# Kernel optimization log

Hardware: AMD Instinct MI355X
Metric: run time of the kernel (lower is better)

## Reference

```python
import jax, jax.numpy as jnp
import numpy as np

B, S, T, D, H, DF = 2, 2048, 2048, 1024, 16, 4096
DK = D // H
EPS = 1e-5


def _linear_params(key, d_in, d_out):
    kw, kb = jax.random.split(key)
    s = 1.0 / np.sqrt(d_in)
    W = jax.random.uniform(kw, (d_out, d_in), jnp.float32, -s, s)
    b = jax.random.uniform(kb, (d_out,), jnp.float32, -s, s)
    return W, b


def setup_inputs() -> dict:
    key = jax.random.key(0)
    ks = jax.random.split(key, 16)
    inp = {}
    inp['x'] = jax.random.normal(ks[0], (B, S, D), jnp.float32)
    inp['enc_out'] = jax.random.normal(ks[1], (B, T, D), jnp.float32)
    inp['src_mask'] = jnp.ones((B, 1, 1, T), jnp.int32)
    inp['tgt_mask'] = jnp.tril(jnp.ones((S, S), jnp.int32))[None, None, :, :]
    # self-attn params
    for i, nm in enumerate(['q1', 'k1', 'v1', 'o1']):
        W, b = _linear_params(ks[2 + i], D, D)
        inp['W' + nm], inp['b' + nm] = W, b
    # cross-attn params
    for i, nm in enumerate(['q2', 'k2', 'v2', 'o2']):
        W, b = _linear_params(ks[6 + i], D, D)
        inp['W' + nm], inp['b' + nm] = W, b
    # FFN
    inp['Wf1'], inp['bf1'] = _linear_params(ks[10], D, DF)
    inp['Wf2'], inp['bf2'] = _linear_params(ks[11], DF, D)
    # LayerNorms
    for i in (1, 2, 3):
        inp[f'g{i}'] = jnp.ones((D,), jnp.float32)
        inp[f'be{i}'] = jnp.zeros((D,), jnp.float32)
    return inp


def _lin(x, W, b):
    return x @ W.T + b


def _ln(x, g, b):
    mu = jnp.mean(x, -1, keepdims=True)
    var = jnp.mean(jnp.square(x - mu), -1, keepdims=True)
    return (x - mu) * jax.lax.rsqrt(var + EPS) * g + b


def _mha(q_in, k_in, v_in, Wq, bq, Wk, bk, Wv, bv, Wo, bo, mask):
    Bq = q_in.shape[0]
    q = _lin(q_in, Wq, bq).reshape(Bq, -1, H, DK).transpose(0, 2, 1, 3)
    k = _lin(k_in, Wk, bk).reshape(Bq, -1, H, DK).transpose(0, 2, 1, 3)
    v = _lin(v_in, Wv, bv).reshape(Bq, -1, H, DK).transpose(0, 2, 1, 3)
    scores = jnp.einsum('bhqd,bhkd->bhqk', q, k) / np.sqrt(DK)
    scores = jnp.where(mask == 0, -jnp.inf, scores)
    attn = jax.nn.softmax(scores, axis=-1)
    out = jnp.einsum('bhqk,bhkd->bhqd', attn, v)
    out = out.transpose(0, 2, 1, 3).reshape(Bq, -1, H * DK)
    return _lin(out, Wo, bo)


def reference(x, enc_out, src_mask, tgt_mask,
              Wq1, bq1, Wk1, bk1, Wv1, bv1, Wo1, bo1,
              Wq2, bq2, Wk2, bk2, Wv2, bv2, Wo2, bo2,
              Wf1, bf1, Wf2, bf2,
              g1, be1, g2, be2, g3, be3):
    out = _mha(x, x, x, Wq1, bq1, Wk1, bk1, Wv1, bv1, Wo1, bo1, tgt_mask)
    x = _ln(x + out, g1, be1)
    out = _mha(x, enc_out, enc_out, Wq2, bq2, Wk2, bk2, Wv2, bv2, Wo2, bo2, src_mask)
    x = _ln(x + out, g2, be2)
    ff = _lin(jax.nn.relu(_lin(x, Wf1, bf1)), Wf2, bf2)
    return _ln(x + ff, g3, be3)
```

## Files before the change

### kernel.cpp

```cpp
#include <hip/hip_runtime.h>


typedef __bf16 bf16_t;
typedef bf16_t  bf16x8 __attribute__((ext_vector_type(8)));
typedef float   f32x4  __attribute__((ext_vector_type(4)));
typedef unsigned short ushort_t;
typedef ushort_t u16x8 __attribute__((ext_vector_type(8)));
typedef ushort_t u16x4 __attribute__((ext_vector_type(4)));

__device__ __forceinline__ float b2f(ushort_t u) {
    union { unsigned u; float f; } x; x.u = ((unsigned)u) << 16; return x.f;
}
__device__ __forceinline__ ushort_t f2b(float f) {
    union { float f; unsigned u; } x; x.f = f;
    unsigned r = x.u + 0x7fffu + ((x.u >> 16) & 1u);
    return (ushort_t)(r >> 16);
}
__device__ __forceinline__ unsigned pk2(float lo, float hi) {
    union { float f; unsigned u; } a, b; a.f = lo; b.f = hi;
    return (b.u & 0xffff0000u) | (a.u >> 16);
}

#if __has_builtin(__builtin_amdgcn_exp2f)
#define EXP2(x) __builtin_amdgcn_exp2f(x)
#else
#define EXP2(x) exp2f(x)
#endif

#define GLL(gp, lp)                                                            \
    __builtin_amdgcn_global_load_lds(                                          \
        (const __attribute__((address_space(1))) void*)(gp),                   \
        (__attribute__((address_space(3))) void*)(lp), 16, 0, 0)

__global__ __launch_bounds__(256) void conv_all(
    const float* __restrict__ x,   const float* __restrict__ enc,
    const float* __restrict__ w0, const float* __restrict__ w1,
    const float* __restrict__ w2, const float* __restrict__ w3,
    const float* __restrict__ w4, const float* __restrict__ w5,
    const float* __restrict__ w6, const float* __restrict__ w7,
    const float* __restrict__ wf1, const float* __restrict__ wf2,
    ushort_t* __restrict__ Xb, ushort_t* __restrict__ Eb,
    ushort_t* __restrict__ Wb)
{
    const int b = blockIdx.x;
    const float* src;
    ushort_t* dst;
    size_t blk;
    if (b < 2048)      { src = x;   dst = Xb; blk = b; }
    else if (b < 4096) { src = enc; dst = Eb; blk = b - 2048; }
    else if (b < 8192) {
        const int i = (b - 4096) >> 9;
        src = (i < 4) ? (i < 2 ? (i == 0 ? w0 : w1) : (i == 2 ? w2 : w3))
                      : (i < 6 ? (i == 4 ? w4 : w5) : (i == 6 ? w6 : w7));
        dst = Wb + (size_t)i * 1048576;
        blk = (b - 4096) & 511;
    }
    else if (b < 10240) { src = wf1; dst = Wb + (size_t)8  * 1048576; blk = b - 8192; }
    else                { src = wf2; dst = Wb + (size_t)12 * 1048576; blk = b - 10240; }

    const size_t e = blk * 2048 + (size_t)threadIdx.x * 8;
    const float4 a = *(const float4*)(src + e);
    const float4 c = *(const float4*)(src + e + 4);
    uint4 r;
    r.x = pk2(a.x, a.y); r.y = pk2(a.z, a.w);
    r.z = pk2(c.x, c.y); r.w = pk2(c.z, c.w);
    *(uint4*)(dst + e) = r;
}

template <int EPI, int TM, bool RF32, bool FUSED, bool SPLITA, bool SPLITC,
          bool TRV, bool QSC>
__global__ __launch_bounds__(256) void gemm_bt(
    const ushort_t* __restrict__ A, const ushort_t* __restrict__ A2,
    const ushort_t* __restrict__ W,
    const float* __restrict__ b1, const float* __restrict__ b2,
    const float* __restrict__ b3,
    const void* __restrict__ Rv,
    ushort_t* __restrict__ C, ushort_t* __restrict__ C2,
    int M, int N, int K)
{
    constexpr int IM = TM / 32;
    __shared__ __align__(16) ushort_t At[TM * 32];
    __shared__ __align__(16) ushort_t Bt[128 * 32];

    const int tid  = threadIdx.x;
    const int lane = tid & 63, w = tid >> 6;
    const int g = lane >> 4, qi = lane & 15;

    const int nbn = gridDim.x, nbm = gridDim.y;
    const int lin = blockIdx.x + nbn * blockIdx.y;
    const int xcd = lin & 7, j = lin >> 3;
    const int bpx = nbm >> 3;
    const int bmb = xcd * bpx + (j & (bpx - 1));
    const int bnb = j / bpx;
    const int bm = bmb * TM, bn = bnb * 128;

    const int wm = (w >> 1) * (TM / 2), wn = (w & 1) * 64;

    const ushort_t* Ap = SPLITA ? ((bm < 2048) ? A : A2) : A;
    const int       am = SPLITA ? (bm & 2047) : bm;

    const int srow = lane >> 2;
    const int scol = (lane & 3) * 8;

    f32x4 acc[IM][4] = {};

    const int niter = K >> 5;
    for (int kt = 0; kt < niter; ++kt) {
        const int k0 = kt << 5;
        __syncthreads();
        if (TM == 128) {
#pragma unroll
            for (int c = 0; c < 2; ++c) {
                const int s = c * 4 + w;
                GLL(Ap + (size_t)(am + s * 16 + srow) * K + k0 + scol, At + s * 512);
            }
        } else {
            GLL(Ap + (size_t)(am + w * 16 + srow) * K + k0 + scol, At + w * 512);
        }
#pragma unroll
        for (int c = 0; c < 2; ++c) {
            const int s = c * 4 + w;
            GLL(W + (size_t)(bn + s * 16 + srow) * K + k0 + scol, Bt + s * 512);
        }
        __syncthreads();

        bf16x8 af[IM], bfr[4];
#pragma unroll
        for (int i = 0; i < IM; ++i)
            af[i] = *(const bf16x8*)(At + (wm + i * 16 + qi) * 32 + g * 8);
#pragma unroll
        for (int j2 = 0; j2 < 4; ++j2)
            bfr[j2] = *(const bf16x8*)(Bt + (wn + j2 * 16 + qi) * 32 + g * 8);
#pragma unroll
        for (int i = 0; i < IM; ++i)
#pragma unroll
            for (int j2 = 0; j2 < 4; ++j2)
                acc[i][j2] = __builtin_amdgcn_mfma_f32_16x16x32_bf16(
                    af[i], bfr[j2], acc[i][j2], 0, 0, 0);
    }

    const float* bp = FUSED ? (bn < 1024 ? b1 : (bn < 2048 ? b2 : b3)) : b1;
#pragma unroll
    for (int j2 = 0; j2 < 4; ++j2) {
        const int n = bn + wn + j2 * 16 + qi;
        const int nl = n & 1023;
        const float bv = bp[nl];
#pragma unroll
        for (int i = 0; i < IM; ++i) {
            if (EPI == 1 && TRV && bn >= N - 1024) {
                const int which = bn >> 10;
                const int h = nl >> 6, dk = nl & 63;
                const int m0 = bm + wm + i * 16 + g * 4;
                const int bb = m0 >> 11, s0 = m0 & 2047;
                u16x4 pv;
#pragma unroll
                for (int r = 0; r < 4; ++r) pv[r] = f2b(acc[i][j2][r] + bv);
                *(u16x4*)(C + (size_t)which * 4194304 +
                          (((size_t)((bb << 4) + h)) * 64 + dk) * 2048 + s0) = pv;
            } else {
#pragma unroll
                for (int r = 0; r < 4; ++r) {
                    const int m = bm + wm + i * 16 + g * 4 + r;
                    float v = acc[i][j2][r] + bv;
                    if (EPI == 2) {
                        v += RF32 ? ((const float*)Rv)[(size_t)m * N + n]
                                  : b2f(((const ushort_t*)Rv)[(size_t)m * N + n]);
                    }
                    if (EPI == 3) v = v > 0.f ? v : 0.f;
                    if (EPI == 1) {
                        const int which = FUSED ? (bn >> 10) : 0;
                        if (QSC && which == 0)
                            v *= 0.18033688011112042f;
                        const int bb = m >> 11, s = m & 2047;
                        const int h = nl >> 6, dk = nl & 63;
                        const size_t dst = (size_t)which * 4194304 +
                            (((size_t)((bb << 4) + h)) * 2048 + s) * 64 + dk;
                        C[dst] = f2b(v);
                    } else {
                        ushort_t* Cp = SPLITC ? (m < 2048 ? C : C2) : C;
                        const int mr = SPLITC ? (m & 2047) : m;
                        Cp[(size_t)mr * N + n] = f2b(v);
                    }
                }
            }
        }
    }
}

template <bool CAUSAL>
__global__ __launch_bounds__(256) void flash_attn(
    const ushort_t* __restrict__ Q, const ushort_t* __restrict__ K,
    const ushort_t* __restrict__ V, ushort_t* __restrict__ O, int S)
{
    __shared__ __align__(16) ushort_t Kt[3][2048];
    __shared__ __align__(16) ushort_t Vt[3][2048];
    __shared__ __align__(16) ushort_t Pl[2048];

    const int tid = threadIdx.x, lane = tid & 63, w = tid >> 6;
    const int g = lane >> 4, qi = lane & 15;
    const int q2 = (qi >> 1) & 3;
    const int bh = blockIdx.x;
    const int y = blockIdx.y;
    const int qb = CAUSAL ? ((y & 8) ? ((y & 16) ? 55 - y : 23 - y) : y) : y;
    const size_t base = (size_t)bh * S * 64;
    const int q0 = qb << 6;
    const int qw = q0 + w * 16;

    const int krow2 = ((w & 1) << 4) + (lane >> 2);
    const int kcol2 = ((w >> 1) << 5) + ((lane & 3) << 3);
    const ushort_t* Kp = K + base + (size_t)krow2 * 64 + kcol2;
    const ushort_t* Vp = V + base + (size_t)(w * 16 + (lane >> 2)) * 2048 +
                         ((lane & 3) << 3);

    bf16x8 qf0 = *(const bf16x8*)(Q + base + (size_t)(qw + qi) * 64 + g * 8);
    bf16x8 qf1 = *(const bf16x8*)(Q + base + (size_t)(qw + qi) * 64 + 32 + g * 8);
    asm volatile("" :: "v"(qf0), "v"(qf1));

    f32x4 oacc[4] = {};
    float lsum = 0.f;

    const int ntiles = CAUSAL ? ((q0 >> 5) + 2) : (S >> 5);

    GLL(Kp, &Kt[0][w * 512]);
    GLL(Vp, &Vt[0][w * 512]);
    GLL(Kp + (size_t)32 * 64, &Kt[1][w * 512]);
    GLL(Vp + 32, &Vt[1][w * 512]);
    asm volatile("s_waitcnt vmcnt(2)" ::: "memory");
    __builtin_amdgcn_s_barrier();
    __builtin_amdgcn_sched_barrier(0);

    int c0 = 0;
    for (int t = 0; t < ntiles; ++t) {
        const bool pre = (t + 2 < ntiles);

        if (pre) {
            const int kn = (t + 2) << 5;
            int cn = c0 + 2; if (cn >= 3) cn -= 3;
            GLL(Kp + (size_t)kn * 64, &Kt[cn][w * 512]);
            GLL(Vp + kn, &Vt[cn][w * 512]);
        }
        __builtin_amdgcn_sched_barrier(0);

        f32x4 st[2] = {};
        __builtin_amdgcn_s_setprio(1);
#pragma unroll
        for (int tt = 0; tt < 2; ++tt) {
            bf16x8 kf0 = *(const bf16x8*)(&Kt[c0][(tt * 16 + qi) * 32 + g * 8]);
            bf16x8 kf1 = *(const bf16x8*)(&Kt[c0][1024 + (tt * 16 + qi) * 32 + g * 8]);
            st[tt] = __builtin_amdgcn_mfma_f32_16x16x32_bf16(kf0, qf0, st[tt], 0, 0, 0);
            st[tt] = __builtin_amdgcn_mfma_f32_16x16x32_bf16(kf1, qf1, st[tt], 0, 0, 0);
        }
        __builtin_amdgcn_s_setprio(0);

        const int k0 = t << 5;
        if (CAUSAL && (k0 + 31 > qw)) {
#pragma unroll
            for (int tt = 0; tt < 2; ++tt)
#pragma unroll
                for (int r = 0; r < 4; ++r)
                    if (k0 + tt * 16 + g * 4 + r > qw + qi) st[tt][r] = -1e30f;
        }

        float p[2][4];
#pragma unroll
        for (int tt = 0; tt < 2; ++tt)
#pragma unroll
            for (int r = 0; r < 4; ++r) {
                p[tt][r] = EXP2(st[tt][r]);
                lsum += p[tt][r];
            }

        ushort_t* pb = Pl + w * 512;
#pragma unroll
        for (int tt = 0; tt < 2; ++tt) {
            unsigned lo, hi;
            asm("v_cvt_pk_bf16_f32 %0, %1, %2" : "=v"(lo) : "v"(p[tt][0]), "v"(p[tt][1]));
            asm("v_cvt_pk_bf16_f32 %0, %1, %2" : "=v"(hi) : "v"(p[tt][2]), "v"(p[tt][3]));
            const int swc = (tt * 2 + (g >> 1)) ^ q2;
            uint2 pw; pw.x = lo; pw.y = hi;
            *(uint2*)(pb + qi * 32 + swc * 8 + (g & 1) * 4) = pw;
        }
        asm volatile("s_waitcnt lgkmcnt(0)" ::: "memory");
        __builtin_amdgcn_sched_barrier(0);
        bf16x8 pf = *(const bf16x8*)(pb + qi * 32 + ((g ^ q2) << 3));

        __builtin_amdgcn_s_setprio(1);
#pragma unroll
        for (int dt = 0; dt < 4; ++dt) {
            bf16x8 vf = *(const bf16x8*)(&Vt[c0][(dt * 16 + qi) * 32 + g * 8]);
            oacc[dt] = __builtin_amdgcn_mfma_f32_16x16x32_bf16(pf, vf, oacc[dt], 0, 0, 0);
        }
        __builtin_amdgcn_s_setprio(0);

        if (pre) {
            asm volatile("s_waitcnt vmcnt(2)" ::: "memory");
        } else {
            asm volatile("s_waitcnt vmcnt(0)" ::: "memory");
        }
        __builtin_amdgcn_s_barrier();
        __builtin_amdgcn_sched_barrier(0);
        if (++c0 == 3) c0 = 0;
    }

    lsum += __shfl_xor(lsum, 16);
    lsum += __shfl_xor(lsum, 32);
    float lv[4];
#pragma unroll
    for (int r = 0; r < 4; ++r) lv[r] = 1.f / __shfl(lsum, g * 4 + r, 16);

    const int b = bh >> 4, h = bh & 15;
#pragma unroll
    for (int dt = 0; dt < 4; ++dt)
#pragma unroll
        for (int r = 0; r < 4; ++r) {
            const int row = b * S + qw + g * 4 + r;
            const int col = (h << 6) + dt * 16 + qi;
            O[(size_t)row * 1024 + col] = f2b(oacc[dt][r] * lv[r]);
        }
}

template <bool OUTF32>
__global__ __launch_bounds__(256) void ln_kernel(
    const ushort_t* __restrict__ X, const float* __restrict__ gam,
    const float* __restrict__ bet, void* __restrict__ Yv)
{
    const int row = blockIdx.x, tid = threadIdx.x;
    const int lane = tid & 63, w = tid >> 6;
    const size_t off = (size_t)row * 1024 + tid * 4;

    u16x4 xv = *(const u16x4*)(X + off);
    float f[4];
#pragma unroll
    for (int i = 0; i < 4; ++i) f[i] = b2f(xv[i]);

    float s = f[0] + f[1] + f[2] + f[3];
    float sq = f[0] * f[0] + f[1] * f[1] + f[2] * f[2] + f[3] * f[3];
#pragma unroll
    for (int o = 32; o; o >>= 1) {
        s  += __shfl_xor(s, o);
        sq += __shfl_xor(sq, o);
    }
    __shared__ float red[8];
    if (lane == 0) { red[w] = s; red[4 + w] = sq; }
    __syncthreads();
    s  = red[0] + red[1] + red[2] + red[3];
    sq = red[4] + red[5] + red[6] + red[7];

    const float mu = s * (1.f / 1024.f);
    const float var = sq * (1.f / 1024.f) - mu * mu;
    const float rs = rsqrtf(var + 1e-5f);

    const float4 gv = *(const float4*)(gam + tid * 4);
    const float4 bv = *(const float4*)(bet + tid * 4);
    float y0 = (f[0] - mu) * rs * gv.x + bv.x;
    float y1 = (f[1] - mu) * rs * gv.y + bv.y;
    float y2 = (f[2] - mu) * rs * gv.z + bv.z;
    float y3 = (f[3] - mu) * rs * gv.w + bv.w;

    if (OUTF32) {
        float4 yv; yv.x = y0; yv.y = y1; yv.z = y2; yv.w = y3;
        *(float4*)((float*)Yv + off) = yv;
    } else {
        u16x4 yv;
        yv[0] = f2b(y0); yv[1] = f2b(y1); yv[2] = f2b(y2); yv[3] = f2b(y3);
        *(u16x4*)((ushort_t*)Yv + off) = yv;
    }
}

extern "C" void kernel_launch(void* const* d_in, const int* in_sizes, int n_in,
                              void* d_out, int out_size, void* d_ws, size_t ws_size,
                              hipStream_t stream)
{
    const float* x   = (const float*)d_in[0];
    const float* enc = (const float*)d_in[1];
    const float* Wq1 = (const float*)d_in[4];
    const float* bq1 = (const float*)d_in[5];
    const float* Wk1 = (const float*)d_in[6];
    const float* bk1 = (const float*)d_in[7];
    const float* Wv1 = (const float*)d_in[8];
    const float* bv1 = (const float*)d_in[9];
    const float* Wo1 = (const float*)d_in[10];
    const float* bo1 = (const float*)d_in[11];
    const float* Wq2 = (const float*)d_in[12];
    const float* bq2 = (const float*)d_in[13];
    const float* Wk2 = (const float*)d_in[14];
    const float* bk2 = (const float*)d_in[15];
    const float* Wv2 = (const float*)d_in[16];
    const float* bv2 = (const float*)d_in[17];
    const float* Wo2 = (const float*)d_in[18];
    const float* bo2 = (const float*)d_in[19];
    const float* Wf1 = (const float*)d_in[20];
    const float* bf1 = (const float*)d_in[21];
    const float* Wf2 = (const float*)d_in[22];
    const float* bf2 = (const float*)d_in[23];
    const float* gm1 = (const float*)d_in[24];
    const float* be1 = (const float*)d_in[25];
    const float* gm2 = (const float*)d_in[26];
    const float* be2 = (const float*)d_in[27];
    const float* gm3 = (const float*)d_in[28];
    const float* be3 = (const float*)d_in[29];

    float*    out = (float*)d_out;
    ushort_t* ws  = (ushort_t*)d_ws;
    ushort_t* F2  = (ushort_t*)d_out;

    const size_t E = (size_t)4096 * 1024;
    ushort_t* P0 = ws;
    ushort_t* P1 = ws + 1 * E;
    ushort_t* P2 = ws + 2 * E;
    ushort_t* P3 = ws + 3 * E;
    ushort_t* P4 = ws + 4 * E;
    ushort_t* Wb = ws + 5 * E;

    const size_t M1 = 1048576;
    ushort_t* Wb_qkv1 = Wb;
    ushort_t* Wb_o1   = Wb + 3 * M1;
    ushort_t* Wb_q2   = Wb + 4 * M1;
    ushort_t* Wb_kv2  = Wb + 5 * M1;
    ushort_t* Wb_o2   = Wb + 7 * M1;
    ushort_t* Wb_f1   = Wb + 8 * M1;
    ushort_t* Wb_f2   = Wb + 12 * M1;

    const dim3 blk(256);
    const dim3 gA(32, 32);

    conv_all<<<12288, blk, 0, stream>>>(x, enc, Wq1, Wk1, Wv1, Wo1, Wq2, Wk2,
                                        Wv2, Wo2, Wf1, Wf2, P3, P4, Wb);

    gemm_bt<1, 128, false, true, false, false, true, true><<<dim3(24, 32), blk, 0, stream>>>(
        P3, nullptr, Wb_qkv1, bq1, bk1, bv1, nullptr, P0, nullptr, 4096, 3072, 1024);
    flash_attn<true><<<gA, blk, 0, stream>>>(P0, P1, P2, P3, 2048);
    gemm_bt<2, 64, true, false, false, false, false, false><<<dim3(8, 64), blk, 0, stream>>>(
        P3, nullptr, Wb_o1, bo1, bo1, bo1, x, P0, nullptr, 4096, 1024, 1024);
    ln_kernel<false><<<4096, blk, 0, stream>>>(P0, gm1, be1, P1);

    gemm_bt<1, 64, false, false, false, false, false, true><<<dim3(8, 64), blk, 0, stream>>>(
        P1, nullptr, Wb_q2, bq2, bq2, bq2, nullptr, P0, nullptr, 4096, 1024, 1024);
    gemm_bt<1, 128, false, true, false, false, true, false><<<dim3(16, 32), blk, 0, stream>>>(
        P4, nullptr, Wb_kv2, bk2, bv2, bv2, nullptr, P2, nullptr, 4096, 2048, 1024);
    flash_attn<false><<<gA, blk, 0, stream>>>(P0, P2, P3, P4, 2048);
    gemm_bt<2, 64, false, false, false, false, false, false><<<dim3(8, 64), blk, 0, stream>>>(
        P4, nullptr, Wb_o2, bo2, bo2, bo2, P1, P0, nullptr, 4096, 1024, 1024);
    ln_kernel<false><<<4096, blk, 0, stream>>>(P0, gm2, be2, P2);

    gemm_bt<3, 128, false, false, false, true, false, false><<<dim3(32, 32), blk, 0, stream>>>(
        P2, nullptr, Wb_f1, bf1, bf1, bf1, nullptr, P0, F2, 4096, 4096, 1024);
    gemm_bt<2, 64, false, false, true, false, false, false><<<dim3(8, 64), blk, 0, stream>>>(
        P0, F2, Wb_f2, bf2, bf2, bf2, P2, P3, nullptr, 4096, 1024, 4096);
    ln_kernel<true><<<4096, blk, 0, stream>>>(P3, gm3, be3, out);
}
```

Baseline: 577.4 us.

## Triple-buffer GEMM LDS tiles with async prefetch two k-steps ahead

Converts the GEMM main loop from a single-buffered load-sync-compute pattern into a three-stage LDS ring. Global-to-LDS loads for tile kt+2 are issued before computing on tile kt, and explicit vmcnt waits plus a single barrier per iteration replace the two __syncthreads. The goal is to hide global memory latency behind MFMA work. The cost is three times the LDS footprint, which may lower occupancy, and correctness now depends on hand-counted vmcnt values.

```diff
diff --git a/kernel.cpp b/kernel.cpp
--- a/kernel.cpp
+++ b/kernel.cpp
@@ -79,8 +79,8 @@
     int M, int N, int K)
 {
     constexpr int IM = TM / 32;
-    __shared__ __align__(16) ushort_t At[TM * 32];
-    __shared__ __align__(16) ushort_t Bt[128 * 32];
+    __shared__ __align__(16) ushort_t At[3][TM * 32];
+    __shared__ __align__(16) ushort_t Bt[3][128 * 32];
 
     const int tid  = threadIdx.x;
     const int lane = tid & 63, w = tid >> 6;
@@ -105,38 +105,70 @@
     f32x4 acc[IM][4] = {};
 
     const int niter = K >> 5;
-    for (int kt = 0; kt < niter; ++kt) {
-        const int k0 = kt << 5;
-        __syncthreads();
-        if (TM == 128) {
-#pragma unroll
-            for (int c = 0; c < 2; ++c) {
-                const int s = c * 4 + w;
-                GLL(Ap + (size_t)(am + s * 16 + srow) * K + k0 + scol, At + s * 512);
+
+    auto stage = [&](int kt, int c) {
+        const int k0s = kt << 5;
+        if constexpr (TM == 128) {
+#pragma unroll
+            for (int cc = 0; cc < 2; ++cc) {
+                const int s = cc * 4 + w;
+                GLL(Ap + (size_t)(am + s * 16 + srow) * K + k0s + scol,
+                    &At[c][s * 512]);
             }
         } else {
-            GLL(Ap + (size_t)(am + w * 16 + srow) * K + k0 + scol, At + w * 512);
-        }
-#pragma unroll
-        for (int c = 0; c < 2; ++c) {
-            const int s = c * 4 + w;
-            GLL(W + (size_t)(bn + s * 16 + srow) * K + k0 + scol, Bt + s * 512);
-        }
-        __syncthreads();
+            GLL(Ap + (size_t)(am + w * 16 + srow) * K + k0s + scol,
+                &At[c][w * 512]);
+        }
+#pragma unroll
+        for (int cc = 0; cc < 2; ++cc) {
+            const int s = cc * 4 + w;
+            GLL(W + (size_t)(bn + s * 16 + srow) * K + k0s + scol,
+                &Bt[c][s * 512]);
+        }
+    };
+
+    stage(0, 0);
+    stage(1, 1);
+    if constexpr (TM == 128) asm volatile("s_waitcnt vmcnt(4)" ::: "memory");
+    else                     asm volatile("s_waitcnt vmcnt(3)" ::: "memory");
+    __builtin_amdgcn_s_barrier();
+    __builtin_amdgcn_sched_barrier(0);
+
+    int c0 = 0;
+    for (int kt = 0; kt < niter; ++kt) {
+        const bool pre = (kt + 2 < niter);
+
+        if (pre) {
+            int cn = c0 + 2; if (cn >= 3) cn -= 3;
+            stage(kt + 2, cn);
+        }
+        __builtin_amdgcn_sched_barrier(0);
 
         bf16x8 af[IM], bfr[4];
 #pragma unroll
         for (int i = 0; i < IM; ++i)
-            af[i] = *(const bf16x8*)(At + (wm + i * 16 + qi) * 32 + g * 8);
+            af[i] = *(const bf16x8*)(&At[c0][(wm + i * 16 + qi) * 32 + g * 8]);
 #pragma unroll
         for (int j2 = 0; j2 < 4; ++j2)
-            bfr[j2] = *(const bf16x8*)(Bt + (wn + j2 * 16 + qi) * 32 + g * 8);
+            bfr[j2] = *(const bf16x8*)(&Bt[c0][(wn + j2 * 16 + qi) * 32 + g * 8]);
 #pragma unroll
         for (int i = 0; i < IM; ++i)
 #pragma unroll
             for (int j2 = 0; j2 < 4; ++j2)
                 acc[i][j2] = __builtin_amdgcn_mfma_f32_16x16x32_bf16(
                     af[i], bfr[j2], acc[i][j2], 0, 0, 0);
+
+        if (pre) {
+            if constexpr (TM == 128)
+                asm volatile("s_waitcnt vmcnt(4)" ::: "memory");
+            else
+                asm volatile("s_waitcnt vmcnt(3)" ::: "memory");
+        } else {
+            asm volatile("s_waitcnt vmcnt(0)" ::: "memory");
+        }
+        __builtin_amdgcn_s_barrier();
+        __builtin_amdgcn_sched_barrier(0);
+        if (++c0 == 3) c0 = 0;
     }
 
     const float* bp = FUSED ? (bn < 1024 ? b1 : (bn < 2048 ? b2 : b3)) : b1;
```

Measured after the change: 563.9 us. 1.02x faster.
